# Performance work log

Measured on AMD Instinct MI355X. Metric: run time of the kernel, lower is better.

## Reference

```python
import jax, jax.numpy as jnp
import numpy as np

N_GENES_TOTAL = 2000
N_FREQ = 50
E_DIM = 10
N_FRAGMENTS = 131072
N_CELLS = 200
N_GENES_MB = 500
ENC_DIM = 4 * N_FREQ  # 200


def setup_inputs() -> dict:
    key = jax.random.key(0)
    k0, k1, k2, k3 = jax.random.split(key, 4)
    # fragment coordinates (start/end positions around the TSS, ~kb scale)
    coordinates = jax.random.normal(k0, (N_FRAGMENTS, 2), dtype=jnp.float32) * 1000.0
    # sorted ragged cell-x-gene segment index (required by segment_*_coo)
    local_cellxgene_ix = jnp.sort(
        jax.random.randint(k1, (N_FRAGMENTS,), 0, N_CELLS * N_GENES_MB)
    )
    # genes of interest in this minibatch (indices into the global gene table)
    genes_oi = jax.random.randint(k2, (N_GENES_MB,), 0, N_GENES_TOTAL)
    # consistent per-fragment gene mapping
    genemapping = genes_oi[local_cellxgene_ix % N_GENES_MB]
    # FragmentEmbedder params
    stdv = 1.0 / np.sqrt(E_DIM)
    W1 = jax.random.uniform(k3, (N_GENES_TOTAL, ENC_DIM, E_DIM), dtype=jnp.float32,
                            minval=-stdv, maxval=stdv)
    b1 = jnp.zeros((N_GENES_TOTAL, E_DIM), dtype=jnp.float32)
    # EmbeddingToExpression params, 'default' init: first 5 ones, rest zero, last -1
    w2 = np.zeros((N_GENES_TOTAL, E_DIM), dtype=np.float32)
    w2[:, :5] = 1.0
    w2[:, -1] = -1.0
    w2 = jnp.asarray(w2)
    b2 = jnp.zeros((N_GENES_TOTAL,), dtype=jnp.float32)
    return dict(coordinates=coordinates, genemapping=genemapping,
                local_cellxgene_ix=local_cellxgene_ix, genes_oi=genes_oi,
                W1=W1, b1=b1, w2=w2, b2=b2, cell_n=N_CELLS, gene_n=N_GENES_MB)


def _sine_encode(coordinates):
    nf = N_FREQ
    i = jnp.arange(1, nf + 1, dtype=coordinates.dtype)
    freqs = jnp.repeat(1.0 / (1000.0 ** (2.0 * i / nf)), 2)            # [2*nf]
    shifts = jnp.tile(jnp.array([0.0, jnp.pi / 2], coordinates.dtype), nf)  # [2*nf]
    # [F,2,1]*[2nf] -> [F,2,2nf] -> flatten last two -> [F, 4*nf]
    enc = jnp.sin((coordinates[..., None] * freqs + shifts)
                  .reshape(coordinates.shape[0], -1))
    return enc


def reference(coordinates, genemapping, local_cellxgene_ix, genes_oi,
              W1, b1, w2, b2, cell_n, gene_n):
    # FragmentEmbedder: sine encoding + per-gene linear + sigmoid
    enc = _sine_encode(coordinates)                                   # [F, 200]
    h = jnp.einsum('fe,feo->fo', enc, W1[genemapping]) + b1[genemapping]  # [F, 10]
    h = jax.nn.sigmoid(h)
    # EmbeddingGenePooler: segment-sum over sorted cellxgene index
    pooled = jax.ops.segment_sum(h, local_cellxgene_ix,
                                 num_segments=cell_n * gene_n,
                                 indices_are_sorted=True)             # [C*G, 10]
    pooled = pooled.reshape(cell_n, gene_n, -1)                       # [C, G, 10]
    # EmbeddingToExpression: per-gene weighted sum + bias
    out = (pooled * w2[genes_oi]).sum(-1) + b2[genes_oi]              # [C, G]
    return out
```

## Files before the change

kernel.cpp:

```cpp
#include <hip/hip_runtime.h>

#define NFRAG   131072
#define NCELLS  200
#define NGENES  500
#define NSEG    (NCELLS * NGENES)
#define EDIM    10
#define NFREQ   50
#define W1_ROW  2000
#define BLOCK   256
#define NWAVE   (BLOCK / 64)
#define CHUNKS  2
#define CPC     (NCELLS / CHUNKS)
#define MAXT    288
#define KSTEPS  7

typedef __attribute__((ext_vector_type(8))) short short8;
typedef __attribute__((ext_vector_type(4))) float float4v;

__device__ inline unsigned short bf16rn(float f) {
    unsigned u = __float_as_uint(f);
    u += 0x7fffu + ((u >> 16) & 1u);
    return (unsigned short)(u >> 16);
}

__global__ __launch_bounds__(256) void bounds_kernel(
    const int* __restrict__ cxg, int* __restrict__ off)
{
    int f = blockIdx.x * 256 + threadIdx.x;
    if (f >= NFRAG) return;
    int cur = cxg[f];
    int nxt = (f + 1 < NFRAG) ? cxg[f + 1] : NSEG;
    if (f == 0)
        for (int s = 0; s <= cur; ++s) off[s] = 0;
    for (int s = cur + 1; s <= nxt; ++s) off[s] = f + 1;
}

__global__ __launch_bounds__(BLOCK) void gene_kernel(
    const float* __restrict__ coords,
    const int*   __restrict__ off,
    const int*   __restrict__ genes_oi,
    const float* __restrict__ W1,
    const float* __restrict__ b1,
    const float* __restrict__ w2,
    const float* __restrict__ b2,
    float* __restrict__ out)
{
    __shared__ __attribute__((aligned(16))) float sW[W1_ROW];
    __shared__ __attribute__((aligned(16))) float2 sCo[MAXT];
    __shared__ float outacc[CPC];
    __shared__ unsigned short fcell[MAXT];
    __shared__ int wtot[NWAVE + 1];

    const int g     = blockIdx.x >> 1;
    const int cbase = (blockIdx.x & 1) * CPC;
    const int t    = threadIdx.x;
    const int lane = t & 63;
    const int wid  = t >> 6;
    const int n    = lane & 15;
    const int qb   = (lane >> 4) * 8;
    const int gg   = genes_oi[g];

    int lo = 0, cnt = 0;
    if (t < CPC) {
        int seg = (cbase + t) * NGENES + g;
        lo  = off[seg];
        cnt = off[seg + 1] - lo;
    }
    const float4* Wg4 = (const float4*)(W1 + (size_t)gg * W1_ROW);
    float4 wst0 = Wg4[t];
    float4 wst1 = Wg4[t + BLOCK];
    ((float4*)sW)[t] = wst0;
    ((float4*)sW)[t + BLOCK] = wst1;
    if (t < CPC) outacc[t] = 0.0f;

    const float b1v = (n < EDIM) ? b1[gg * EDIM + n] : 0.0f;
    const float w2v = (n < EDIM) ? w2[gg * EDIM + n] : 0.0f;

    int x = cnt;
    #pragma unroll
    for (int d = 1; d < 64; d <<= 1) {
        int y = __shfl_up(x, d, 64);
        if (lane >= d) x += y;
    }
    if (lane == 63) wtot[wid] = x;
    __syncthreads();
    if (t == 0) {
        int s = 0;
        #pragma unroll
        for (int w = 0; w < NWAVE; ++w) { int v = wtot[w]; wtot[w] = s; s += v; }
        wtot[NWAVE] = s;
    }
    __syncthreads();
    int base = wtot[wid] + (x - cnt);
    const int Tfull = wtot[NWAVE];
    const int T = (Tfull < MAXT) ? Tfull : MAXT;

    for (int i = 0; i < cnt; ++i) {
        int slot = base + i;
        if (slot < MAXT) {
            sCo[slot] = ((const float2*)coords)[lo + i];
            fcell[slot] = (unsigned short)t;
        }
    }

    short8 Bf[KSTEPS];
    #pragma unroll
    for (int ks = 0; ks < KSTEPS; ++ks) {
        short8 bv;
        #pragma unroll
        for (int j = 0; j < 8; ++j) {
            int e = qb + j + 32 * ks;
            float w = (e < 200 && n < EDIM) ? sW[e * EDIM + n] : 0.0f;
            bv[j] = (short)bf16rn(w);
        }
        Bf[ks] = bv;
    }

    float fr[KSTEPS * 4];
    #pragma unroll
    for (int ks = 0; ks < KSTEPS; ++ks) {
        #pragma unroll
        for (int p = 0; p < 4; ++p) {
            int e0 = qb + 32 * ks + 2 * p;
            int jj = e0; if (jj >= 200) jj -= 200; if (jj >= 100) jj -= 100;
            int kf = jj >> 1;
            fr[ks * 4 + p] = exp2f(-(float)(kf + 1) * (9.965784284662087f / 25.0f));
        }
    }
    __syncthreads();

    const int tiles = (T + 15) >> 4;
    for (int tile = wid; tile < tiles; tile += NWAVE) {
        const int tb = tile << 4;
        int i = tb + n;
        if (i >= T) i = T - 1;
        float2 co = sCo[i];

        float4v acc = { b1v, b1v, b1v, b1v };

        #pragma unroll
        for (int ks = 0; ks < KSTEPS; ++ks) {
            short8 a;
            #pragma unroll
            for (int p = 0; p < 4; ++p) {
                int e0 = qb + 32 * ks + 2 * p;
                float xv = ((e0 >= 100) ? co.y : co.x) * fr[ks * 4 + p];
                float nn = rintf(xv * 0.15915494309189535f);
                float r = fmaf(nn, -6.28125f, xv);
                r = fmaf(nn, -0.0019353071795864769f, r);
                a[2 * p]     = (short)bf16rn(__sinf(r));
                a[2 * p + 1] = (short)bf16rn(__cosf(r));
            }
            acc = __builtin_amdgcn_mfma_f32_16x16x32_bf16(a, Bf[ks], acc, 0, 0, 0);
        }

        #pragma unroll
        for (int r = 0; r < 4; ++r) {
            float h = 1.0f / (1.0f + __expf(-acc[r]));
            float sv = h * w2v;
            sv += __shfl_xor(sv, 1);
            sv += __shfl_xor(sv, 2);
            sv += __shfl_xor(sv, 4);
            sv += __shfl_xor(sv, 8);
            int row = (lane >> 4) * 4 + r;
            int idx = tb + row;
            if (n == 0 && idx < T) {
                atomicAdd(&outacc[fcell[idx]], sv);
            }
        }
    }
    __syncthreads();

    if (t < CPC) out[(cbase + t) * NGENES + g] = outacc[t] + b2[gg];
}

extern "C" void kernel_launch(void* const* d_in, const int* in_sizes, int n_in,
                              void* d_out, int out_size, void* d_ws, size_t ws_size,
                              hipStream_t stream)
{
    const float* coords   = (const float*)d_in[0];
    const int*   cxg      = (const int*)  d_in[2];
    const int*   genes_oi = (const int*)  d_in[3];
    const float* W1       = (const float*)d_in[4];
    const float* b1       = (const float*)d_in[5];
    const float* w2       = (const float*)d_in[6];
    const float* b2       = (const float*)d_in[7];
    float* out = (float*)d_out;
    int*   off = (int*)d_ws;

    bounds_kernel<<<(NFRAG + 255) / 256, 256, 0, stream>>>(cxg, off);
    gene_kernel<<<NGENES * CHUNKS, BLOCK, 0, stream>>>(coords, off, genes_oi,
                                                       W1, b1, w2, b2, out);
}
```

Measured before the change: 100.5 us.

## Fuse segment-bounds computation into gene kernel via binary search and use hardware sin/cos

Removes the separate bounds kernel that built a segment offset table in workspace. Instead, each block binary-searches the sorted cellxgene index for its own segment boundaries, which saves a launch and the global offset writes and reads. It also changes the sine encoding to compute phase in revolutions, using fract and the native amdgcn sin/cos builtins, and packs bf16 pairs directly. The trade-off is about 17 dependent cached global loads per thread for the search, plus slightly different trig precision.

```diff
diff --git a/kernel.cpp b/kernel.cpp
--- a/kernel.cpp
+++ b/kernel.cpp
@@ -5,7 +5,6 @@
 #define NGENES  500
 #define NSEG    (NCELLS * NGENES)
 #define EDIM    10
-#define NFREQ   50
 #define W1_ROW  2000
 #define BLOCK   256
 #define NWAVE   (BLOCK / 64)
@@ -23,21 +22,9 @@
     return (unsigned short)(u >> 16);
 }
 
-__global__ __launch_bounds__(256) void bounds_kernel(
-    const int* __restrict__ cxg, int* __restrict__ off)
-{
-    int f = blockIdx.x * 256 + threadIdx.x;
-    if (f >= NFRAG) return;
-    int cur = cxg[f];
-    int nxt = (f + 1 < NFRAG) ? cxg[f + 1] : NSEG;
-    if (f == 0)
-        for (int s = 0; s <= cur; ++s) off[s] = 0;
-    for (int s = cur + 1; s <= nxt; ++s) off[s] = f + 1;
-}
-
 __global__ __launch_bounds__(BLOCK) void gene_kernel(
     const float* __restrict__ coords,
-    const int*   __restrict__ off,
+    const int*   __restrict__ cxg,
     const int*   __restrict__ genes_oi,
     const float* __restrict__ W1,
     const float* __restrict__ b1,
@@ -50,6 +37,7 @@
     __shared__ float outacc[CPC];
     __shared__ unsigned short fcell[MAXT];
     __shared__ int wtot[NWAVE + 1];
+    __shared__ int sB[2 * CPC];
 
     const int g     = blockIdx.x >> 1;
     const int cbase = (blockIdx.x & 1) * CPC;
@@ -60,21 +48,35 @@
     const int qb   = (lane >> 4) * 8;
     const int gg   = genes_oi[g];
 
-    int lo = 0, cnt = 0;
-    if (t < CPC) {
-        int seg = (cbase + t) * NGENES + g;
-        lo  = off[seg];
-        cnt = off[seg + 1] - lo;
-    }
     const float4* Wg4 = (const float4*)(W1 + (size_t)gg * W1_ROW);
     float4 wst0 = Wg4[t];
     float4 wst1 = Wg4[t + BLOCK];
+
+    if (t < 2 * CPC) {
+        const int target = (cbase + (t >> 1)) * NGENES + g + (t & 1);
+        int pos = 0;
+        #pragma unroll
+        for (int half = NFRAG; half >= 1; half >>= 1) {
+            int cand = pos + half;
+            if (cand <= NFRAG && cxg[cand - 1] < target) pos = cand;
+        }
+        sB[t] = pos;
+    }
+
     ((float4*)sW)[t] = wst0;
     ((float4*)sW)[t + BLOCK] = wst1;
     if (t < CPC) outacc[t] = 0.0f;
 
     const float b1v = (n < EDIM) ? b1[gg * EDIM + n] : 0.0f;
     const float w2v = (n < EDIM) ? w2[gg * EDIM + n] : 0.0f;
+
+    __syncthreads();
+
+    int lo = 0, cnt = 0;
+    if (t < CPC) {
+        lo  = sB[2 * t];
+        cnt = sB[2 * t + 1] - lo;
+    }
 
     int x = cnt;
     #pragma unroll
@@ -116,7 +118,7 @@
         Bf[ks] = bv;
     }
 
-    float fr[KSTEPS * 4];
+    float fr2[KSTEPS * 4];
     #pragma unroll
     for (int ks = 0; ks < KSTEPS; ++ks) {
         #pragma unroll
@@ -124,7 +126,8 @@
             int e0 = qb + 32 * ks + 2 * p;
             int jj = e0; if (jj >= 200) jj -= 200; if (jj >= 100) jj -= 100;
             int kf = jj >> 1;
-            fr[ks * 4 + p] = exp2f(-(float)(kf + 1) * (9.965784284662087f / 25.0f));
+            fr2[ks * 4 + p] = exp2f(-(float)(kf + 1) * (9.965784284662087f / 25.0f))
+                              * 0.15915494309189535f;
         }
     }
     __syncthreads();
@@ -140,18 +143,28 @@
 
         #pragma unroll
         for (int ks = 0; ks < KSTEPS; ++ks) {
-            short8 a;
+            union { short8 s8; unsigned u[4]; } A;
             #pragma unroll
             for (int p = 0; p < 4; ++p) {
                 int e0 = qb + 32 * ks + 2 * p;
-                float xv = ((e0 >= 100) ? co.y : co.x) * fr[ks * 4 + p];
-                float nn = rintf(xv * 0.15915494309189535f);
-                float r = fmaf(nn, -6.28125f, xv);
-                r = fmaf(nn, -0.0019353071795864769f, r);
-                a[2 * p]     = (short)bf16rn(__sinf(r));
-                a[2 * p + 1] = (short)bf16rn(__cosf(r));
+                float sel = (e0 >= 100) ? co.y : co.x;
+                float rev = sel * fr2[ks * 4 + p];
+#if __has_builtin(__builtin_amdgcn_fractf)
+                float fv = __builtin_amdgcn_fractf(rev);
+#else
+                float fv = rev - floorf(rev);
+#endif
+#if __has_builtin(__builtin_amdgcn_sinf)
+                float sv = __builtin_amdgcn_sinf(fv);
+                float cv = __builtin_amdgcn_cosf(fv);
+#else
+                float sv = __sinf(fv * 6.283185307179586f);
+                float cv = __cosf(fv * 6.283185307179586f);
+#endif
+                A.u[p] = (unsigned)bf16rn(sv)
+                       | ((unsigned)bf16rn(cv) << 16);
             }
-            acc = __builtin_amdgcn_mfma_f32_16x16x32_bf16(a, Bf[ks], acc, 0, 0, 0);
+            acc = __builtin_amdgcn_mfma_f32_16x16x32_bf16(A.s8, Bf[ks], acc, 0, 0, 0);
         }
 
         #pragma unroll
@@ -186,9 +199,8 @@
     const float* w2       = (const float*)d_in[6];
     const float* b2       = (const float*)d_in[7];
     float* out = (float*)d_out;
-    int*   off = (int*)d_ws;
-
-    bounds_kernel<<<(NFRAG + 255) / 256, 256, 0, stream>>>(cxg, off);
-    gene_kernel<<<NGENES * CHUNKS, BLOCK, 0, stream>>>(coords, off, genes_oi,
+    (void)d_ws; (void)ws_size;
+
+    gene_kernel<<<NGENES * CHUNKS, BLOCK, 0, stream>>>(coords, cxg, genes_oi,
                                                        W1, b1, w2, b2, out);
 }
```

New measurement: 102.7 us. +2.3%, slower.
